# Performance work log

Hardware: AMD Instinct MI355X
Metric: run time of the kernel (lower is better)

Reference implementation:

```python
import jax, jax.numpy as jnp
import numpy as np

DATA_DIM = 128
UNITS = 512
LAYERS = 3
BATCH = 32
IN_STEPS = 1000   # int((T_input + 0.5*dt)//dt)
OUT_STEPS = 100   # int((T_output + 0.5*dt)//dt)


def setup_inputs() -> dict:
    key = jax.random.key(0)
    ks = jax.random.split(key, 16)
    d = {}
    d["x"] = jax.random.normal(ks[0], (BATCH, IN_STEPS, DATA_DIM), jnp.float32)
    in_dims = [DATA_DIM, UNITS, UNITS]
    i = 1
    for j in range(LAYERS):
        d[f"W{j}"] = jax.random.normal(ks[i], (in_dims[j], 3 * UNITS), jnp.float32) * 0.05; i += 1
        d[f"U{j}"] = jax.random.normal(ks[i], (UNITS, 3 * UNITS), jnp.float32) * 0.05; i += 1
        d[f"b{j}"] = jnp.zeros((2, 3 * UNITS), jnp.float32)
        d[f"s{j}"] = jax.random.normal(ks[i], (1, UNITS), jnp.float32); i += 1
    d["Wd"] = jax.random.normal(ks[i], (UNITS, DATA_DIM), jnp.float32) * 0.05
    d["bd"] = jnp.zeros((DATA_DIM,), jnp.float32)
    return d


def _gru_cell(x, h, W, U, b):
    # Keras GRUCell, reset_after=True (TF2 default)
    mx = x @ W + b[0]           # [B, 3U]
    mh = h @ U + b[1]           # [B, 3U]
    xz, xr, xh = jnp.split(mx, 3, axis=-1)
    hz, hr, hh = jnp.split(mh, 3, axis=-1)
    z = jax.nn.sigmoid(xz + hz)
    r = jax.nn.sigmoid(xr + hr)
    cand = jnp.tanh(xh + r * hh)
    return z * h + (1.0 - z) * cand


def reference(x, W0, U0, b0, s0, W1, U1, b1, s1, W2, U2, b2, s2, Wd, bd):
    params = [(W0, U0, b0), (W1, U1, b1), (W2, U2, b2)]
    B = x.shape[0]
    # learnable initial states, tiled over batch -> [L, B, U]
    h0 = jnp.stack([jnp.tile(s, (B, 1)) for s in (s0, s1, s2)])
    # model processes timesteps 0 .. in_steps-2 (last input step unused)
    xs = jnp.swapaxes(x[:, : IN_STEPS - 1, :], 0, 1)  # [T-1, B, D]

    def step(h, xt):
        hs = []
        inp = xt
        for j, (W, U, b) in enumerate(params):
            hj = _gru_cell(inp, h[j], W, U, b)
            hs.append(hj)
            inp = hj
        hn = jnp.stack(hs)  # [L, B, U]
        return hn, (inp, hn)

    _, (ys, hs) = jax.lax.scan(step, h0, xs)
    # outputs correspond to steps in_steps-out_steps-1 .. in_steps-2
    ys = ys[-OUT_STEPS:]   # [out_steps, B, U]
    hs = hs[-OUT_STEPS:]   # [out_steps, L, B, U]
    preds = ys @ Wd + bd   # [out_steps, B, D]
    predictions = jnp.swapaxes(preds, 0, 1)        # [B, out_steps, D]
    hidden = jnp.transpose(hs, (2, 0, 1, 3))       # [B, out_steps, L, U]
    return predictions, hidden
```

## Files before the change

kernel.cpp:

```cpp
#include <hip/hip_runtime.h>
#include <math.h>

#define B_   32
#define INS  1000
#define TS   999
#define D_   128
#define U_   512
#define G3   1536
#define OUTS 100
#define NB   208
#define NTHR 512

#define HBUF_OFF 0
#define HBUF_SZ  (4*3*512*32)
#define RING_OFF HBUF_SZ
#define RING_SZ  (4*1536*32)
#define BAR_OFF  (RING_OFF + RING_SZ)

#define SMEM_FLOATS 36864
#define PIDX4(s,g,c,e) ((((s)*4+(g))*8+(c))*36 + (e))
#define XBUF_OFF 12288

#define WT_STORE(p, v) __hip_atomic_store((p), (v), __ATOMIC_RELAXED, __HIP_MEMORY_SCOPE_AGENT)
#define CG_LOAD(p)     __hip_atomic_load((p), __ATOMIC_RELAXED, __HIP_MEMORY_SCOPE_AGENT)

#define GLOAD_LDS(G, L) __builtin_amdgcn_global_load_lds( \
  (const __attribute__((address_space(1))) void*)(G), \
  (__attribute__((address_space(3))) void*)(L), 16, 0, 0)

#define WAITVN(N) do { asm volatile("s_waitcnt vmcnt(" #N ")" ::: "memory"); \
  __builtin_amdgcn_sched_barrier(0); } while (0)
#define WAIT_FOR(C, NCH) do { \
  if ((NCH) - 1 - (C) >= 5)      { WAITVN(5); } \
  else if ((NCH) - 1 - (C) == 4) { WAITVN(4); } \
  else if ((NCH) - 1 - (C) == 3) { WAITVN(3); } \
  else if ((NCH) - 1 - (C) == 2) { WAITVN(2); } \
  else if ((NCH) - 1 - (C) == 1) { WAITVN(1); } \
  else                           { WAITVN(0); } } while (0)

#define CHUNK_FMA8(C, GH) { \
  const float* bp  = stg + ((C) % 6) * 2048 + sub * 256 + eg * 4; \
  const float* wp2 = smem + ((C) * 64 + sub * 8) * 24 + c_l * 3; \
  _Pragma("unroll") \
  for (int rr = 0; rr < 8; ++rr) { \
    float4 av = *(const float4*)(bp + rr * 32); \
    float w0 = wp2[0], w1 = wp2[1], w2 = wp2[2]; \
    az[0]=fmaf(av.x,w0,az[0]); az[1]=fmaf(av.y,w0,az[1]); \
    az[2]=fmaf(av.z,w0,az[2]); az[3]=fmaf(av.w,w0,az[3]); \
    ar[0]=fmaf(av.x,w1,ar[0]); ar[1]=fmaf(av.y,w1,ar[1]); \
    ar[2]=fmaf(av.z,w1,ar[2]); ar[3]=fmaf(av.w,w1,ar[3]); \
    GH[0]=fmaf(av.x,w2,GH[0]); GH[1]=fmaf(av.y,w2,GH[1]); \
    GH[2]=fmaf(av.z,w2,GH[2]); GH[3]=fmaf(av.w,w2,GH[3]); \
    wp2 += 24; \
  } }

#define ISSUE_CHUNK(SRCBASE, CC) do { \
  const float* gsrc_ = (SRCBASE) + wv * 256 + lane * 4; \
  GLOAD_LDS(gsrc_, stg + ((CC) % 6) * 2048 + wv * 256); \
} while (0)

__global__ void gru_init_kernel(const float* __restrict__ s0,
                                const float* __restrict__ s1,
                                const float* __restrict__ s2,
                                float* __restrict__ ws) {
  int g = blockIdx.x * 256 + threadIdx.x;
  if (g < 4096) { unsigned* bar = (unsigned*)(ws + BAR_OFF); bar[g] = 0u; }
  for (int i = g; i < 3 * 512 * 32; i += gridDim.x * 256) {
    int which = i / (512 * 32);
    int r = i - which * (512 * 32);
    int k = r >> 5, e = r & 31;
    const float* s = (which == 0) ? s0 : ((which == 1) ? s1 : s2);
    ws[HBUF_OFF + 3 * 49152 + which * 16384 + k * 32 + e] = s[k];
  }
}

__device__ __forceinline__ void wait_deps(unsigned* slots, int role, int t) {
  const int tid = threadIdx.x;
  const unsigned* p = nullptr; int tgt = 0;
  if (role < 0) {
    if (tid < 64)       { p = &slots[(0   + tid)       * 16]; tgt = t - 3; }
  } else if (role == 0) {
    if (tid < 64)       { p = &slots[(0   + tid)       * 16]; tgt = t;     }
    else if (tid < 80)  { p = &slots[(192 + tid - 64)  * 16]; tgt = t + 1; }
    else if (tid < 144) { p = &slots[(64  + tid - 80)  * 16]; tgt = t - 3; }
  } else if (role == 1) {
    if (tid < 64)       { p = &slots[(64  + tid)       * 16]; tgt = t;     }
    else if (tid < 128) { p = &slots[(0   + tid - 64)  * 16]; tgt = t + 1; }
    else if (tid < 192) { p = &slots[(128 + tid - 128) * 16]; tgt = t - 3; }
  } else {
    if (tid < 64)       { p = &slots[(128 + tid)       * 16]; tgt = t;     }
    else if (tid < 128) { p = &slots[(64  + tid - 64)  * 16]; tgt = t + 1; }
  }
  if (p && tgt > 0) {
    while ((int)CG_LOAD(p) < tgt) __builtin_amdgcn_s_sleep(1);
  }
  __syncthreads();
  if (role >= 0) {
    if (threadIdx.x == 0) __builtin_amdgcn_fence(__ATOMIC_ACQUIRE, "agent");
    __syncthreads();
  }
}

__device__ __forceinline__ void publish(unsigned* slots, int sidx, int t) {
  __syncthreads();
  if (threadIdx.x == 0) WT_STORE(&slots[sidx * 16], (unsigned)(t + 1));
}

__global__ __launch_bounds__(NTHR, 1) void gru_persist(
    const float* __restrict__ x,
    const float* __restrict__ W0c, const float* __restrict__ U0c, const float* __restrict__ b0c,
    const float* __restrict__ W1c, const float* __restrict__ U1c, const float* __restrict__ b1c,
    const float* __restrict__ W2c, const float* __restrict__ U2c, const float* __restrict__ b2c,
    const float* __restrict__ Wd, const float* __restrict__ bd,
    float* __restrict__ out, float* __restrict__ ws)
{
  float* hbuf = ws + HBUF_OFF;
  float* ring = ws + RING_OFF;
  unsigned* slots = (unsigned*)(ws + BAR_OFF);
  float* pred_out = out;
  float* hid_out  = out + B_ * OUTS * D_;

  const int bid = blockIdx.x;
  const int tid = threadIdx.x;

  int role, rb;
  if      (bid < 16)  { role = -1; rb = bid; }
  else if (bid < 80)  { role = 0;  rb = bid - 16; }
  else if (bid < 144) { role = 1;  rb = bid - 80; }
  else                { role = 2;  rb = bid - 144; }
  const int sidx = (role < 0) ? (192 + rb) : (role * 64 + rb);

  __shared__ float smem[SMEM_FLOATS];
  float* stg  = smem + ((role == 0) ? 12288 : 24576);
  float* part = stg;

  const int eg  = tid & 7;
  const int c_l = (tid >> 3) & 7;
  const int sub = tid >> 6;
  const int wv  = tid >> 6;
  const int lane = tid & 63;
  const int cb  = (rb & 7) * 8 + (rb >> 3);
  const int c0  = cb * 8;
  const int rc = tid >> 5;
  const int re = tid & 31;
  const int xb0 = ((rb & 7) * 2 + (rb >> 3)) * 96;
  const int cg3 = (tid & 31) * 3;
  const int e0  = (tid >> 5) * 2;

  const float *Wj = nullptr, *Ujp = nullptr, *bj = nullptr;
  if      (role == 0) { Ujp = U0c; bj = b0c; }
  else if (role == 1) { Wj = W1c; Ujp = U1c; bj = b1c; }
  else if (role == 2) { Wj = W2c; Ujp = U2c; bj = b2c; }

  if (role < 0) {
    for (int idx = tid; idx < 128 * 96; idx += NTHR)
      smem[idx] = W0c[(idx / 96) * G3 + xb0 + (idx % 96)];
    for (int f = tid; f < 1024; f += NTHR) {
      int e = f >> 5, d4 = (f & 31) * 4;
      *(float4*)(smem + XBUF_OFF + e * 128 + d4) =
          *(const float4*)(x + e * (INS * D_) + d4);
    }
  } else if (role == 0) {
    for (int idx = tid; idx < 512 * 24; idx += NTHR) {
      int row = idx / 24, cg = idx - row * 24, cc = cg / 3, g = cg - cc * 3;
      smem[idx] = Ujp[row * G3 + g * 512 + c0 + cc];
    }
  } else {
    for (int idx = tid; idx < 1024 * 24; idx += NTHR) {
      int row = idx / 24, cg = idx - row * 24, cc = cg / 3, g = cg - cc * 3;
      const float* mat = (row < 512) ? Wj : Ujp;
      int mr = (row < 512) ? row : row - 512;
      smem[idx] = mat[mr * G3 + g * 512 + c0 + cc];
    }
  }
  float bz = 0.f, br = 0.f, b0h = 0.f, b1h = 0.f;
  if (role >= 0 && tid < 256) {
    const int cg2 = c0 + rc;
    bz  = bj[cg2] + bj[G3 + cg2];
    br  = bj[512 + cg2] + bj[G3 + 512 + cg2];
    b0h = bj[1024 + cg2];
    b1h = bj[G3 + 1024 + cg2];
  }
  __syncthreads();

  for (int t = 0; t < TS; ++t) {
    wait_deps(slots, role, t);

    if (role < 0) {
      float4 xp0, xp1;
      const bool pf = (t + 1) < TS;
      if (pf) {
        int f0 = tid, f1 = tid + 512;
        xp0 = *(const float4*)(x + (f0 >> 5) * (INS * D_) + (t + 1) * D_ + (f0 & 31) * 4);
        xp1 = *(const float4*)(x + (f1 >> 5) * (INS * D_) + (t + 1) * D_ + (f1 & 31) * 4);
      }
      const float* xb = smem + XBUF_OFF + (t & 1) * 4096;
      float acc[3][2];
      #pragma unroll
      for (int c = 0; c < 3; ++c) { acc[c][0] = 0.f; acc[c][1] = 0.f; }
      #pragma unroll 4
      for (int k4 = 0; k4 < D_; k4 += 4) {
        float4 v0 = *(const float4*)(xb + e0 * 128 + k4);
        float4 v1 = *(const float4*)(xb + (e0 + 1) * 128 + k4);
        float xs0[4] = {v0.x, v0.y, v0.z, v0.w};
        float xs1[4] = {v1.x, v1.y, v1.z, v1.w};
        #pragma unroll
        for (int kk = 0; kk < 4; ++kk) {
          const float* wpx = smem + (k4 + kk) * 96 + cg3;
          float w0 = wpx[0], w1 = wpx[1], w2 = wpx[2];
          acc[0][0] = fmaf(xs0[kk], w0, acc[0][0]);
          acc[0][1] = fmaf(xs1[kk], w0, acc[0][1]);
          acc[1][0] = fmaf(xs0[kk], w1, acc[1][0]);
          acc[1][1] = fmaf(xs1[kk], w1, acc[1][1]);
          acc[2][0] = fmaf(xs0[kk], w2, acc[2][0]);
          acc[2][1] = fmaf(xs1[kk], w2, acc[2][1]);
        }
      }
      float* dst = ring + (t & 3) * (G3 * 32);
      #pragma unroll
      for (int c = 0; c < 3; ++c) {
        WT_STORE(dst + (xb0 + cg3 + c) * 32 + e0,     acc[c][0]);
        WT_STORE(dst + (xb0 + cg3 + c) * 32 + e0 + 1, acc[c][1]);
      }
      if (pf) {
        float* xw = smem + XBUF_OFF + ((t + 1) & 1) * 4096;
        int f0 = tid, f1 = tid + 512;
        *(float4*)(xw + (f0 >> 5) * 128 + (f0 & 31) * 4) = xp0;
        *(float4*)(xw + (f1 >> 5) * 128 + (f1 & 31) * 4) = xp1;
      }
    } else {
      const int j = role;
      const float* hownb = hbuf + ((t + 3) & 3) * 49152 + j * 16384;
      const float* hupb  = (j > 0) ? (hbuf + (t & 3) * 49152 + (j - 1) * 16384)
                                   : nullptr;

      float az[4] = {0,0,0,0}, ar[4] = {0,0,0,0};
      float axh[4] = {0,0,0,0}, ahh[4] = {0,0,0,0};

      if (j == 0) {
        ISSUE_CHUNK(hownb + 0 * 2048, 0); ISSUE_CHUNK(hownb + 1 * 2048, 1);
        ISSUE_CHUNK(hownb + 2 * 2048, 2); ISSUE_CHUNK(hownb + 3 * 2048, 3);
        ISSUE_CHUNK(hownb + 4 * 2048, 4); ISSUE_CHUNK(hownb + 5 * 2048, 5);
        #pragma unroll
        for (int c = 0; c < 8; ++c) {
          WAIT_FOR(c, 8);
          CHUNK_FMA8(c, ahh);
          __builtin_amdgcn_sched_barrier(0);
          if (c + 6 < 8) ISSUE_CHUNK(hownb + (c + 6) * 2048, c + 6);
        }
      } else {
        ISSUE_CHUNK(hupb + 0 * 2048, 0); ISSUE_CHUNK(hupb + 1 * 2048, 1);
        ISSUE_CHUNK(hupb + 2 * 2048, 2); ISSUE_CHUNK(hupb + 3 * 2048, 3);
        ISSUE_CHUNK(hupb + 4 * 2048, 4); ISSUE_CHUNK(hupb + 5 * 2048, 5);
        #pragma unroll
        for (int c = 0; c < 16; ++c) {
          WAIT_FOR(c, 16);
          if (c < 8) { CHUNK_FMA8(c, axh); } else { CHUNK_FMA8(c, ahh); }
          __builtin_amdgcn_sched_barrier(0);
          if (c + 6 < 16) {
            const int cc = c + 6;
            const float* nsrc = (cc < 8) ? (hupb + cc * 2048)
                                         : (hownb + (cc - 8) * 2048);
            ISSUE_CHUNK(nsrc, cc);
          }
        }
      }

      float xz = 0.f, xr2 = 0.f, xhv0 = 0.f, hp = 0.f;
      if (tid < 256) {
        const int cg2 = c0 + rc;
        hp = hownb[cg2 * 32 + re];
        if (j == 0) {
          const float* r3 = ring + (t & 3) * (G3 * 32);
          xz   = r3[cg2 * 32 + re];
          xr2  = r3[(512 + cg2) * 32 + re];
          xhv0 = r3[(1024 + cg2) * 32 + re];
        }
      }

      __syncthreads();

      *(float4*)&part[PIDX4(sub, 0, c_l, eg * 4)] = make_float4(az[0], az[1], az[2], az[3]);
      *(float4*)&part[PIDX4(sub, 1, c_l, eg * 4)] = make_float4(ar[0], ar[1], ar[2], ar[3]);
      if (j == 0) {
        *(float4*)&part[PIDX4(sub, 2, c_l, eg * 4)] = make_float4(ahh[0], ahh[1], ahh[2], ahh[3]);
      } else {
        *(float4*)&part[PIDX4(sub, 2, c_l, eg * 4)] = make_float4(axh[0], axh[1], axh[2], axh[3]);
        *(float4*)&part[PIDX4(sub, 3, c_l, eg * 4)] = make_float4(ahh[0], ahh[1], ahh[2], ahh[3]);
      }
      __syncthreads();

      if (tid < 256) {
        float gz = 0.f, gr = 0.f, xh = 0.f, hh = 0.f;
        #pragma unroll
        for (int s2 = 0; s2 < 8; ++s2) {
          gz += part[PIDX4(s2, 0, rc, re)];
          gr += part[PIDX4(s2, 1, rc, re)];
          if (j == 0) {
            hh += part[PIDX4(s2, 2, rc, re)];
          } else {
            xh += part[PIDX4(s2, 2, rc, re)];
            hh += part[PIDX4(s2, 3, rc, re)];
          }
        }
        const int cg2 = c0 + rc;
        const float xhv = (j == 0) ? xhv0 : xh;
        const float zi = gz + xz + bz;
        const float ri = gr + xr2 + br;
        const float z = 1.f / (1.f + expf(-zi));
        const float r = 1.f / (1.f + expf(-ri));
        const float cand = tanhf((xhv + b0h) + r * (hh + b1h));
        const float hn = z * hp + (1.f - z) * cand;
        WT_STORE(&hbuf[(t & 3) * 49152 + j * 16384 + cg2 * 32 + re], hn);
        if (t >= TS - OUTS) {
          WT_STORE(&hid_out[((re * OUTS + (t - (TS - OUTS))) * 3 + j) * U_ + cg2], hn);
        }
      }
    }
    publish(slots, sidx, t);
  }

  if (tid < 64) {
    while ((int)CG_LOAD(&slots[(128 + tid) * 16]) < TS) __builtin_amdgcn_s_sleep(1);
  }
  __syncthreads();
  if (tid == 0) __builtin_amdgcn_fence(__ATOMIC_ACQUIRE, "agent");
  __syncthreads();

  const int gt = bid * NTHR + tid;
  for (int o = gt; o < B_ * OUTS * D_; o += NB * NTHR) {
    int b  = o / (OUTS * D_);
    int r2 = o - b * (OUTS * D_);
    int s  = r2 >> 7;
    int dd = r2 & 127;
    const float* ys = hid_out + ((b * OUTS + s) * 3 + 2) * U_;
    float acc = bd[dd];
    #pragma unroll 4
    for (int k = 0; k < U_; k += 4) {
      float4 yv = *(const float4*)(ys + k);
      acc = fmaf(yv.x, Wd[(k    ) * D_ + dd], acc);
      acc = fmaf(yv.y, Wd[(k + 1) * D_ + dd], acc);
      acc = fmaf(yv.z, Wd[(k + 2) * D_ + dd], acc);
      acc = fmaf(yv.w, Wd[(k + 3) * D_ + dd], acc);
    }
    pred_out[o] = acc;
  }
}

extern "C" void kernel_launch(void* const* d_in, const int* in_sizes, int n_in,
                              void* d_out, int out_size, void* d_ws, size_t ws_size,
                              hipStream_t stream) {
  const float* x  = (const float*)d_in[0];
  const float* W0 = (const float*)d_in[1];
  const float* U0 = (const float*)d_in[2];
  const float* b0 = (const float*)d_in[3];
  const float* s0 = (const float*)d_in[4];
  const float* W1 = (const float*)d_in[5];
  const float* U1 = (const float*)d_in[6];
  const float* b1 = (const float*)d_in[7];
  const float* s1 = (const float*)d_in[8];
  const float* W2 = (const float*)d_in[9];
  const float* U2 = (const float*)d_in[10];
  const float* b2 = (const float*)d_in[11];
  const float* s2 = (const float*)d_in[12];
  const float* Wd = (const float*)d_in[13];
  const float* bd = (const float*)d_in[14];
  float* ws = (float*)d_ws;

  gru_init_kernel<<<192, 256, 0, stream>>>(s0, s1, s2, ws);
  gru_persist<<<NB, NTHR, 0, stream>>>(x, W0, U0, b0, W1, U1, b1,
                                       W2, U2, b2, Wd, bd, (float*)d_out, ws);
}
```

Before: 9.714 ms.

## Exchange hidden states between blocks in bf16 and keep own state in registers

Hidden states passed between blocks through global memory are now stored as packed bf16 (two values per 32-bit store via v_cvt_pk_bf16_f32), which halves the bytes streamed into LDS each timestep and halves the number of chunk loads per step. Each thread also keeps its own previous hidden value in a register, initialised from s, so it no longer re-reads it from global memory. This cuts latency on the serial per-step critical path. In exchange, the recurrent matmul inputs lose precision, and rounding error can accumulate over the roughly thousand recurrent steps.

```diff
diff --git a/kernel.cpp b/kernel.cpp
--- a/kernel.cpp
+++ b/kernel.cpp
@@ -11,11 +11,10 @@
 #define NB   208
 #define NTHR 512
 
-#define HBUF_OFF 0
-#define HBUF_SZ  (4*3*512*32)
-#define RING_OFF HBUF_SZ
+#define RING_OFF 98304
 #define RING_SZ  (4*1536*32)
 #define BAR_OFF  (RING_OFF + RING_SZ)
+#define HB16PAR  49152
 
 #define SMEM_FLOATS 36864
 #define PIDX4(s,g,c,e) ((((s)*4+(g))*8+(c))*36 + (e))
@@ -38,25 +37,29 @@
   else if ((NCH) - 1 - (C) == 1) { WAITVN(1); } \
   else                           { WAITVN(0); } } while (0)
 
-#define CHUNK_FMA8(C, GH) { \
-  const float* bp  = stg + ((C) % 6) * 2048 + sub * 256 + eg * 4; \
-  const float* wp2 = smem + ((C) * 64 + sub * 8) * 24 + c_l * 3; \
+#define CHUNK_FMA16(C, GH) { \
+  const char* bp  = stgB + ((C) % 6) * 8192 + (sub * 16) * 64 + eg * 8; \
+  const float* wp2 = smem + ((C) * 128 + sub * 16) * 24 + c_l * 3; \
   _Pragma("unroll") \
-  for (int rr = 0; rr < 8; ++rr) { \
-    float4 av = *(const float4*)(bp + rr * 32); \
+  for (int rr = 0; rr < 16; ++rr) { \
+    uint2 uu = *(const uint2*)(bp + rr * 64); \
+    float avx = __uint_as_float(uu.x << 16); \
+    float avy = __uint_as_float(uu.x & 0xFFFF0000u); \
+    float avz = __uint_as_float(uu.y << 16); \
+    float avw = __uint_as_float(uu.y & 0xFFFF0000u); \
     float w0 = wp2[0], w1 = wp2[1], w2 = wp2[2]; \
-    az[0]=fmaf(av.x,w0,az[0]); az[1]=fmaf(av.y,w0,az[1]); \
-    az[2]=fmaf(av.z,w0,az[2]); az[3]=fmaf(av.w,w0,az[3]); \
-    ar[0]=fmaf(av.x,w1,ar[0]); ar[1]=fmaf(av.y,w1,ar[1]); \
-    ar[2]=fmaf(av.z,w1,ar[2]); ar[3]=fmaf(av.w,w1,ar[3]); \
-    GH[0]=fmaf(av.x,w2,GH[0]); GH[1]=fmaf(av.y,w2,GH[1]); \
-    GH[2]=fmaf(av.z,w2,GH[2]); GH[3]=fmaf(av.w,w2,GH[3]); \
+    az[0]=fmaf(avx,w0,az[0]); az[1]=fmaf(avy,w0,az[1]); \
+    az[2]=fmaf(avz,w0,az[2]); az[3]=fmaf(avw,w0,az[3]); \
+    ar[0]=fmaf(avx,w1,ar[0]); ar[1]=fmaf(avy,w1,ar[1]); \
+    ar[2]=fmaf(avz,w1,ar[2]); ar[3]=fmaf(avw,w1,ar[3]); \
+    GH[0]=fmaf(avx,w2,GH[0]); GH[1]=fmaf(avy,w2,GH[1]); \
+    GH[2]=fmaf(avz,w2,GH[2]); GH[3]=fmaf(avw,w2,GH[3]); \
     wp2 += 24; \
   } }
 
-#define ISSUE_CHUNK(SRCBASE, CC) do { \
-  const float* gsrc_ = (SRCBASE) + wv * 256 + lane * 4; \
-  GLOAD_LDS(gsrc_, stg + ((CC) % 6) * 2048 + wv * 256); \
+#define ISSUE_CHUNK(BASEB, CIDX, SLOT) do { \
+  GLOAD_LDS((BASEB) + (CIDX) * 8192 + wv * 1024 + lane * 16, \
+            stgB + ((SLOT) % 6) * 8192 + wv * 1024); \
 } while (0)
 
 __global__ void gru_init_kernel(const float* __restrict__ s0,
@@ -65,12 +68,15 @@
                                 float* __restrict__ ws) {
   int g = blockIdx.x * 256 + threadIdx.x;
   if (g < 4096) { unsigned* bar = (unsigned*)(ws + BAR_OFF); bar[g] = 0u; }
+  unsigned short* hb16 = (unsigned short*)ws;
   for (int i = g; i < 3 * 512 * 32; i += gridDim.x * 256) {
     int which = i / (512 * 32);
     int r = i - which * (512 * 32);
     int k = r >> 5, e = r & 31;
     const float* s = (which == 0) ? s0 : ((which == 1) ? s1 : s2);
-    ws[HBUF_OFF + 3 * 49152 + which * 16384 + k * 32 + e] = s[k];
+    unsigned u = __float_as_uint(s[k]);
+    unsigned b = (u + 0x7FFFu + ((u >> 16) & 1u)) >> 16;
+    hb16[3 * HB16PAR + which * 16384 + k * 32 + e] = (unsigned short)b;
   }
 }
 
@@ -111,10 +117,11 @@
     const float* __restrict__ W0c, const float* __restrict__ U0c, const float* __restrict__ b0c,
     const float* __restrict__ W1c, const float* __restrict__ U1c, const float* __restrict__ b1c,
     const float* __restrict__ W2c, const float* __restrict__ U2c, const float* __restrict__ b2c,
+    const float* __restrict__ s0, const float* __restrict__ s1, const float* __restrict__ s2,
     const float* __restrict__ Wd, const float* __restrict__ bd,
     float* __restrict__ out, float* __restrict__ ws)
 {
-  float* hbuf = ws + HBUF_OFF;
+  unsigned short* hb16 = (unsigned short*)ws;
   float* ring = ws + RING_OFF;
   unsigned* slots = (unsigned*)(ws + BAR_OFF);
   float* pred_out = out;
@@ -132,6 +139,7 @@
 
   __shared__ float smem[SMEM_FLOATS];
   float* stg  = smem + ((role == 0) ? 12288 : 24576);
+  char*  stgB = (char*)stg;
   float* part = stg;
 
   const int eg  = tid & 7;
@@ -147,10 +155,10 @@
   const int cg3 = (tid & 31) * 3;
   const int e0  = (tid >> 5) * 2;
 
-  const float *Wj = nullptr, *Ujp = nullptr, *bj = nullptr;
-  if      (role == 0) { Ujp = U0c; bj = b0c; }
-  else if (role == 1) { Wj = W1c; Ujp = U1c; bj = b1c; }
-  else if (role == 2) { Wj = W2c; Ujp = U2c; bj = b2c; }
+  const float *Wj = nullptr, *Ujp = nullptr, *bj = nullptr, *sj = nullptr;
+  if      (role == 0) { Ujp = U0c; bj = b0c; sj = s0; }
+  else if (role == 1) { Wj = W1c; Ujp = U1c; bj = b1c; sj = s1; }
+  else if (role == 2) { Wj = W2c; Ujp = U2c; bj = b2c; sj = s2; }
 
   if (role < 0) {
     for (int idx = tid; idx < 128 * 96; idx += NTHR)
@@ -173,13 +181,14 @@
       smem[idx] = mat[mr * G3 + g * 512 + c0 + cc];
     }
   }
-  float bz = 0.f, br = 0.f, b0h = 0.f, b1h = 0.f;
+  float bz = 0.f, br = 0.f, b0h = 0.f, b1h = 0.f, hp = 0.f;
   if (role >= 0 && tid < 256) {
     const int cg2 = c0 + rc;
     bz  = bj[cg2] + bj[G3 + cg2];
     br  = bj[512 + cg2] + bj[G3 + 512 + cg2];
     b0h = bj[1024 + cg2];
     b1h = bj[G3 + 1024 + cg2];
+    hp  = sj[cg2];
   }
   __syncthreads();
 
@@ -230,52 +239,41 @@
       }
     } else {
       const int j = role;
-      const float* hownb = hbuf + ((t + 3) & 3) * 49152 + j * 16384;
-      const float* hupb  = (j > 0) ? (hbuf + (t & 3) * 49152 + (j - 1) * 16384)
-                                   : nullptr;
+      const char* ownB = (const char*)(hb16 + ((t + 3) & 3) * HB16PAR + j * 16384);
+      const char* upB  = (j > 0) ? (const char*)(hb16 + (t & 3) * HB16PAR + (j - 1) * 16384)
+                                 : nullptr;
 
       float az[4] = {0,0,0,0}, ar[4] = {0,0,0,0};
       float axh[4] = {0,0,0,0}, ahh[4] = {0,0,0,0};
 
       if (j == 0) {
-        ISSUE_CHUNK(hownb + 0 * 2048, 0); ISSUE_CHUNK(hownb + 1 * 2048, 1);
-        ISSUE_CHUNK(hownb + 2 * 2048, 2); ISSUE_CHUNK(hownb + 3 * 2048, 3);
-        ISSUE_CHUNK(hownb + 4 * 2048, 4); ISSUE_CHUNK(hownb + 5 * 2048, 5);
+        ISSUE_CHUNK(ownB, 0, 0); ISSUE_CHUNK(ownB, 1, 1);
+        ISSUE_CHUNK(ownB, 2, 2); ISSUE_CHUNK(ownB, 3, 3);
+        #pragma unroll
+        for (int c = 0; c < 4; ++c) {
+          WAIT_FOR(c, 4);
+          CHUNK_FMA16(c, ahh);
+        }
+      } else {
+        ISSUE_CHUNK(upB, 0, 0);  ISSUE_CHUNK(upB, 1, 1);
+        ISSUE_CHUNK(upB, 2, 2);  ISSUE_CHUNK(upB, 3, 3);
+        ISSUE_CHUNK(ownB, 0, 4); ISSUE_CHUNK(ownB, 1, 5);
         #pragma unroll
         for (int c = 0; c < 8; ++c) {
           WAIT_FOR(c, 8);
-          CHUNK_FMA8(c, ahh);
+          if (c < 4) { CHUNK_FMA16(c, axh); } else { CHUNK_FMA16(c, ahh); }
           __builtin_amdgcn_sched_barrier(0);
-          if (c + 6 < 8) ISSUE_CHUNK(hownb + (c + 6) * 2048, c + 6);
-        }
-      } else {
-        ISSUE_CHUNK(hupb + 0 * 2048, 0); ISSUE_CHUNK(hupb + 1 * 2048, 1);
-        ISSUE_CHUNK(hupb + 2 * 2048, 2); ISSUE_CHUNK(hupb + 3 * 2048, 3);
-        ISSUE_CHUNK(hupb + 4 * 2048, 4); ISSUE_CHUNK(hupb + 5 * 2048, 5);
-        #pragma unroll
-        for (int c = 0; c < 16; ++c) {
-          WAIT_FOR(c, 16);
-          if (c < 8) { CHUNK_FMA8(c, axh); } else { CHUNK_FMA8(c, ahh); }
-          __builtin_amdgcn_sched_barrier(0);
-          if (c + 6 < 16) {
-            const int cc = c + 6;
-            const float* nsrc = (cc < 8) ? (hupb + cc * 2048)
-                                         : (hownb + (cc - 8) * 2048);
-            ISSUE_CHUNK(nsrc, cc);
-          }
-        }
-      }
-
-      float xz = 0.f, xr2 = 0.f, xhv0 = 0.f, hp = 0.f;
-      if (tid < 256) {
+          if (c + 6 < 8) ISSUE_CHUNK(ownB, (c + 6) - 4, c + 6);
+        }
+      }
+
+      float xz = 0.f, xr2 = 0.f, xhv0 = 0.f;
+      if (tid < 256 && j == 0) {
         const int cg2 = c0 + rc;
-        hp = hownb[cg2 * 32 + re];
-        if (j == 0) {
-          const float* r3 = ring + (t & 3) * (G3 * 32);
-          xz   = r3[cg2 * 32 + re];
-          xr2  = r3[(512 + cg2) * 32 + re];
-          xhv0 = r3[(1024 + cg2) * 32 + re];
-        }
+        const float* r3 = ring + (t & 3) * (G3 * 32);
+        xz   = r3[cg2 * 32 + re];
+        xr2  = r3[(512 + cg2) * 32 + re];
+        xhv0 = r3[(1024 + cg2) * 32 + re];
       }
 
       __syncthreads();
@@ -311,7 +309,15 @@
         const float r = 1.f / (1.f + expf(-ri));
         const float cand = tanhf((xhv + b0h) + r * (hh + b1h));
         const float hn = z * hp + (1.f - z) * cand;
-        WT_STORE(&hbuf[(t & 3) * 49152 + j * 16384 + cg2 * 32 + re], hn);
+        hp = hn;
+        float hnn = __shfl_down(hn, 1);
+        unsigned pk;
+        asm("v_cvt_pk_bf16_f32 %0, %1, %2" : "=v"(pk) : "v"(hn), "v"(hnn));
+        if ((re & 1) == 0) {
+          unsigned* dst16 = (unsigned*)hb16 +
+              (((t & 3) * HB16PAR) + j * 16384 + cg2 * 32 + re) / 2;
+          WT_STORE(dst16, pk);
+        }
         if (t >= TS - OUTS) {
           WT_STORE(&hid_out[((re * OUTS + (t - (TS - OUTS))) * 3 + j) * U_ + cg2], hn);
         }
@@ -369,5 +375,6 @@
 
   gru_init_kernel<<<192, 256, 0, stream>>>(s0, s1, s2, ws);
   gru_persist<<<NB, NTHR, 0, stream>>>(x, W0, U0, b0, W1, U1, b1,
-                                       W2, U2, b2, Wd, bd, (float*)d_out, ws);
-}
+                                       W2, U2, b2, s0, s1, s2,
+                                       Wd, bd, (float*)d_out, ws);
+}
```

Result: slower. 10.25 ms (+5.5%).
